# Performance work log

Hardware: AMD Instinct MI355X
Metric: run time of the kernel (lower is better)

The kernel has to match this reference:

```python
import jax, jax.numpy as jnp
import numpy as np

COMMITMENT_COST = 0.25
EMBEDDING_COST = 1.0


def setup_inputs() -> dict:
    key = jax.random.key(0)
    k1, k2 = jax.random.split(key)
    x = jax.random.normal(k1, (64, 1024, 64), dtype=jnp.float32)
    embeddings = jax.random.normal(k2, (1024, 64), dtype=jnp.float32)
    return {"x": x, "embeddings": embeddings}


def reference(x, embeddings):
    D = embeddings.shape[1]
    flat_x = x.reshape(-1, D)  # [N, D]
    distances = (
        jnp.sum(flat_x ** 2, axis=1, keepdims=True)
        + jnp.sum(embeddings ** 2, axis=1)
        - 2.0 * flat_x @ embeddings.T
    )
    encoding_indices = jnp.argmin(distances, axis=1)  # [N]
    quantized = embeddings[encoding_indices].reshape(x.shape)
    q_latent_loss = jnp.mean((quantized - jax.lax.stop_gradient(x)) ** 2) * EMBEDDING_COST
    e_latent_loss = jnp.mean((x - jax.lax.stop_gradient(quantized)) ** 2) * COMMITMENT_COST
    loss = q_latent_loss + e_latent_loss
    # Straight-through estimator
    quantized_st = x + jax.lax.stop_gradient(quantized - x)
    return (quantized_st, loss)
```

## Files before the change

kernel.cpp:

```cpp
#include <hip/hip_runtime.h>
#include <math.h>

#define NROWS 65536
#define D 64
#define K 1024
#define BR 128
#define EC 128
#define NCH 8
#define THREADS 256
#define TAU_S 0.005f
#define LOSS_SCALE (1.25f / (65536.0f * 64.0f))

typedef short bf16x8 __attribute__((ext_vector_type(8)));
typedef float f32x4 __attribute__((ext_vector_type(4)));

__device__ inline unsigned short f2bf(float f) {
    unsigned int u = __float_as_uint(f);
    unsigned int r = u + 0x7fffu + ((u >> 16) & 1u);
    return (unsigned short)(r >> 16);
}
__device__ inline float bf2f(unsigned short h) {
    return __uint_as_float(((unsigned int)h) << 16);
}
__device__ inline void cvt8(const float4& a, const float4& b, bf16x8& h, bf16x8& l) {
    float f[8] = {a.x, a.y, a.z, a.w, b.x, b.y, b.z, b.w};
#pragma unroll
    for (int j = 0; j < 8; ++j) {
        unsigned short hb = f2bf(f[j]);
        h[j] = (short)hb;
        l[j] = (short)f2bf(f[j] - bf2f(hb));
    }
}

#define MFMA __builtin_amdgcn_mfma_f32_16x16x32_bf16

__global__ void vq_prep(const float* __restrict__ E, float* __restrict__ Ch,
                        bf16x8* __restrict__ Eswz, float* __restrict__ lossp) {
    int k = blockIdx.x * blockDim.x + threadIdx.x;
    if (k == 0) *lossp = 0.f;
    if (k >= K) return;
    const float4* ev = (const float4*)(E + (size_t)k * D);
    float4 v4[16];
    float s = 0.f;
#pragma unroll
    for (int p = 0; p < 16; ++p) {
        float4 v = ev[p];
        v4[p] = v;
        s = fmaf(v.x, v.x, s); s = fmaf(v.y, v.y, s);
        s = fmaf(v.z, v.z, s); s = fmaf(v.w, v.w, s);
    }
    Ch[k] = 0.5f * s;
    int ch = k >> 7, c = k & 127, cs = c & 7;
    size_t base = (size_t)ch * 2048 + c * 8;
#pragma unroll
    for (int u8 = 0; u8 < 8; ++u8) {
        bf16x8 h, l;
        cvt8(v4[2 * u8], v4[2 * u8 + 1], h, l);
        Eswz[base + (u8 ^ cs)] = h;
        Eswz[base + 1024 + (u8 ^ cs)] = l;
    }
}

__global__ __launch_bounds__(THREADS, 2) void vq_main(
    const float* __restrict__ X, const float* __restrict__ E,
    const float* __restrict__ Chg, const bf16x8* __restrict__ Eswz,
    float* __restrict__ out, float* __restrict__ lossp)
{
    __shared__ bf16x8 sBuf[2][2048];
    __shared__ float  sCh[K];
    __shared__ int    sIdx[BR];
    __shared__ int    sFlag[BR];
    __shared__ int    sNf;
    __shared__ float  sLoss[4];

    const int t    = threadIdx.x;
    const int w    = t >> 6;
    const int lane = t & 63;
    const int l15  = lane & 15;
    const int l4   = lane >> 4;
    const int cs   = l15 & 7;
    const int o0   = l4 ^ cs;
    const int o1   = (4 + l4) ^ cs;

    const float4* Xg4 = (const float4*)X;
    const float4* Eg4 = (const float4*)E;

    if (t == 0) sNf = 0;
#pragma unroll
    for (int p = 0; p < 4; ++p) sCh[p * 256 + t] = Chg[p * 256 + t];

    bf16x8 ah[2][2], al[2][2];
#pragma unroll
    for (int rt = 0; rt < 2; ++rt) {
        size_t ab = ((size_t)blockIdx.x * BR + w * 32 + rt * 16 + l15) * 16;
#pragma unroll
        for (int kt = 0; kt < 2; ++kt) {
            float4 fa = Xg4[ab + kt * 8 + l4 * 2];
            float4 fb = Xg4[ab + kt * 8 + l4 * 2 + 1];
            cvt8(fa, fb, ah[rt][kt], al[rt][kt]);
        }
    }

    bf16x8 rs[8];
#pragma unroll
    for (int p = 0; p < 8; ++p) rs[p] = Eswz[p * 256 + t];
#pragma unroll
    for (int p = 0; p < 8; ++p) sBuf[0][p * 256 + t] = rs[p];
    __syncthreads();

    float m[2][4], m2[2][4]; int bk[2][4];
#pragma unroll
    for (int rt = 0; rt < 2; ++rt)
#pragma unroll
        for (int r = 0; r < 4; ++r) { m[rt][r] = -INFINITY; m2[rt][r] = -INFINITY; bk[rt][r] = 0; }

    for (int ch = 0; ch < NCH; ++ch) {
        const int cur = ch & 1;
        if (ch + 1 < NCH) {
#pragma unroll
            for (int p = 0; p < 8; ++p)
                rs[p] = Eswz[(size_t)(ch + 1) * 2048 + p * 256 + t];
        }
        const bf16x8* __restrict__ bufH = sBuf[cur];
        const bf16x8* __restrict__ bufL = sBuf[cur] + 1024;

#pragma unroll
        for (int g = 0; g < 4; ++g) {
            const int c0 = g * 32 + l15;
            const int c1 = c0 + 16;
            float ce0 = sCh[ch * EC + c0];
            float ce1 = sCh[ch * EC + c1];
            bf16x8 bh00 = bufH[c0 * 8 + o0];
            bf16x8 bh01 = bufH[c0 * 8 + o1];
            bf16x8 bl00 = bufL[c0 * 8 + o0];
            bf16x8 bl01 = bufL[c0 * 8 + o1];
            bf16x8 bh10 = bufH[c1 * 8 + o0];
            bf16x8 bh11 = bufH[c1 * 8 + o1];
            bf16x8 bl10 = bufL[c1 * 8 + o0];
            bf16x8 bl11 = bufL[c1 * 8 + o1];

            f32x4 a00 = {-ce0, -ce0, -ce0, -ce0};
            f32x4 a01 = {-ce0, -ce0, -ce0, -ce0};
            f32x4 a10 = {-ce1, -ce1, -ce1, -ce1};
            f32x4 a11 = {-ce1, -ce1, -ce1, -ce1};

            __builtin_amdgcn_s_setprio(1);
            a00 = MFMA(ah[0][0], bh00, a00, 0, 0, 0); a01 = MFMA(ah[1][0], bh00, a01, 0, 0, 0);
            a10 = MFMA(ah[0][0], bh10, a10, 0, 0, 0); a11 = MFMA(ah[1][0], bh10, a11, 0, 0, 0);
            a00 = MFMA(ah[0][1], bh01, a00, 0, 0, 0); a01 = MFMA(ah[1][1], bh01, a01, 0, 0, 0);
            a10 = MFMA(ah[0][1], bh11, a10, 0, 0, 0); a11 = MFMA(ah[1][1], bh11, a11, 0, 0, 0);
            a00 = MFMA(al[0][0], bh00, a00, 0, 0, 0); a01 = MFMA(al[1][0], bh00, a01, 0, 0, 0);
            a10 = MFMA(al[0][0], bh10, a10, 0, 0, 0); a11 = MFMA(al[1][0], bh10, a11, 0, 0, 0);
            a00 = MFMA(al[0][1], bh01, a00, 0, 0, 0); a01 = MFMA(al[1][1], bh01, a01, 0, 0, 0);
            a10 = MFMA(al[0][1], bh11, a10, 0, 0, 0); a11 = MFMA(al[1][1], bh11, a11, 0, 0, 0);
            a00 = MFMA(ah[0][0], bl00, a00, 0, 0, 0); a01 = MFMA(ah[1][0], bl00, a01, 0, 0, 0);
            a10 = MFMA(ah[0][0], bl10, a10, 0, 0, 0); a11 = MFMA(ah[1][0], bl10, a11, 0, 0, 0);
            a00 = MFMA(ah[0][1], bl01, a00, 0, 0, 0); a01 = MFMA(ah[1][1], bl01, a01, 0, 0, 0);
            a10 = MFMA(ah[0][1], bl11, a10, 0, 0, 0); a11 = MFMA(ah[1][1], bl11, a11, 0, 0, 0);
            __builtin_amdgcn_s_setprio(0);

            const int k0 = ch * EC + c0;
            const int k1 = ch * EC + c1;
#pragma unroll
            for (int r = 0; r < 4; ++r) {
                float v;
                v = a00[r];
                m2[0][r] = fmaxf(m2[0][r], fminf(m[0][r], v));
                bk[0][r] = (v > m[0][r]) ? k0 : bk[0][r];
                m[0][r]  = fmaxf(m[0][r], v);
                v = a01[r];
                m2[1][r] = fmaxf(m2[1][r], fminf(m[1][r], v));
                bk[1][r] = (v > m[1][r]) ? k0 : bk[1][r];
                m[1][r]  = fmaxf(m[1][r], v);
                v = a10[r];
                m2[0][r] = fmaxf(m2[0][r], fminf(m[0][r], v));
                bk[0][r] = (v > m[0][r]) ? k1 : bk[0][r];
                m[0][r]  = fmaxf(m[0][r], v);
                v = a11[r];
                m2[1][r] = fmaxf(m2[1][r], fminf(m[1][r], v));
                bk[1][r] = (v > m[1][r]) ? k1 : bk[1][r];
                m[1][r]  = fmaxf(m[1][r], v);
            }
        }

        if (ch + 1 < NCH) {
#pragma unroll
            for (int p = 0; p < 8; ++p) sBuf[cur ^ 1][p * 256 + t] = rs[p];
        }
        __syncthreads();
    }

#pragma unroll
    for (int rt = 0; rt < 2; ++rt)
#pragma unroll
        for (int r = 0; r < 4; ++r) {
            float mm = m[rt][r], mm2 = m2[rt][r]; int kk = bk[rt][r];
#pragma unroll
            for (int off = 1; off < 16; off <<= 1) {
                float om  = __shfl_xor(mm,  off, 64);
                float om2 = __shfl_xor(mm2, off, 64);
                int   ok  = __shfl_xor(kk,  off, 64);
                mm2 = fmaxf(fmaxf(mm2, om2), fminf(mm, om));
                if (om > mm || (om == mm && ok < kk)) { mm = om; kk = ok; }
            }
            if (l15 == 0) {
                int lr = w * 32 + rt * 16 + l4 * 4 + r;
                sIdx[lr] = kk;
                if (mm - mm2 < TAU_S) {
                    int pos = atomicAdd(&sNf, 1);
                    sFlag[pos] = lr;
                }
            }
        }
    __syncthreads();

    {
        int nf = sNf;
        for (int i = w; i < nf; i += 4) {
            int lr = sFlag[i];
            size_t grow = (size_t)blockIdx.x * BR + lr;
            const float4* xr = Xg4 + grow * 16;
            float bs = -INFINITY; int bki = 0;
#pragma unroll 1
            for (int jj = 0; jj < 16; ++jj) {
                int kq = jj * 64 + lane;
                const float4* er = Eg4 + (size_t)kq * 16;
                float a0 = 0.f, a1 = 0.f, a2 = 0.f, a3 = 0.f;
#pragma unroll
                for (int p = 0; p < 16; p += 4) {
                    float4 xv0 = xr[p],     e0 = er[p];
                    float4 xv1 = xr[p + 1], e1 = er[p + 1];
                    float4 xv2 = xr[p + 2], e2 = er[p + 2];
                    float4 xv3 = xr[p + 3], e3 = er[p + 3];
                    a0 = fmaf(xv0.x, e0.x, a0); a0 = fmaf(xv0.y, e0.y, a0);
                    a0 = fmaf(xv0.z, e0.z, a0); a0 = fmaf(xv0.w, e0.w, a0);
                    a1 = fmaf(xv1.x, e1.x, a1); a1 = fmaf(xv1.y, e1.y, a1);
                    a1 = fmaf(xv1.z, e1.z, a1); a1 = fmaf(xv1.w, e1.w, a1);
                    a2 = fmaf(xv2.x, e2.x, a2); a2 = fmaf(xv2.y, e2.y, a2);
                    a2 = fmaf(xv2.z, e2.z, a2); a2 = fmaf(xv2.w, e2.w, a2);
                    a3 = fmaf(xv3.x, e3.x, a3); a3 = fmaf(xv3.y, e3.y, a3);
                    a3 = fmaf(xv3.z, e3.z, a3); a3 = fmaf(xv3.w, e3.w, a3);
                }
                float sv = ((a0 + a1) + (a2 + a3)) - sCh[kq];
                if (sv > bs) { bs = sv; bki = kq; }
            }
#pragma unroll
            for (int off = 1; off < 64; off <<= 1) {
                float ob = __shfl_xor(bs, off, 64);
                int  okk = __shfl_xor(bki, off, 64);
                if (ob > bs || (ob == bs && okk < bki)) { bs = ob; bki = okk; }
            }
            if (lane == 0) sIdx[lr] = bki;
        }
    }
    __syncthreads();

    {
        int row = t >> 1, half = t & 1;
        int kb = sIdx[row];
        size_t grow = (size_t)blockIdx.x * BR + row;
        const float4* eq   = Eg4 + (size_t)kb * 16;
        const float4* xrow = Xg4 + grow * 16;
        float4* orow = (float4*)out + grow * 16;
        float ls = 0.f;
#pragma unroll
        for (int j = 0; j < 8; ++j) {
            int u = half * 8 + j;
            float4 qv = eq[u];
            float4 xv = xrow[u];
            orow[u] = qv;
            float dx = qv.x - xv.x; ls = fmaf(dx, dx, ls);
            float dy = qv.y - xv.y; ls = fmaf(dy, dy, ls);
            float dz = qv.z - xv.z; ls = fmaf(dz, dz, ls);
            float dw = qv.w - xv.w; ls = fmaf(dw, dw, ls);
        }
#pragma unroll
        for (int off = 32; off > 0; off >>= 1) ls += __shfl_down(ls, off, 64);
        if (lane == 0) sLoss[w] = ls;
        __syncthreads();
        if (t == 0)
            atomicAdd(lossp, (sLoss[0] + sLoss[1] + sLoss[2] + sLoss[3]) * LOSS_SCALE);
    }
}

extern "C" void kernel_launch(void* const* d_in, const int* in_sizes, int n_in,
                              void* d_out, int out_size, void* d_ws, size_t ws_size,
                              hipStream_t stream) {
    const float* X = (const float*)d_in[0];
    const float* E = (const float*)d_in[1];
    float* out   = (float*)d_out;
    float* lossp = out + (size_t)NROWS * D;

    float*  Ch   = (float*)d_ws;
    bf16x8* Eswz = (bf16x8*)((float*)d_ws + 1024);

    vq_prep<<<(K + 255) / 256, 256, 0, stream>>>(E, Ch, Eswz, lossp);

    vq_main<<<NROWS / BR, THREADS, 0, stream>>>(
        X, E, Ch, Eswz, out, lossp);
}
```

Measured before the change: 72.34 us.

## Stream MFMA-fragment-ordered codebook from global memory, split codebook across waves

The prep kernel now writes the bf16 hi/lo codebook directly in per-lane MFMA fragment order, so the main kernel loads B operands straight from global/L2 instead of staging chunks through double-buffered LDS with barriers. Block rows drop to 64 and each pair of waves splits the 1024 codes in half, merging top-1/top-2 through small LDS arrays; occupancy hint rises to 4 blocks. Per-block loss reduction becomes a per-wave atomic. This removes LDS traffic and per-chunk syncs but relies on L2 bandwidth for the codebook reads, doubles the number of blocks re-reading it, and increases global atomics on the loss.

```diff
diff --git a/kernel.cpp b/kernel.cpp
--- a/kernel.cpp
+++ b/kernel.cpp
@@ -4,9 +4,7 @@
 #define NROWS 65536
 #define D 64
 #define K 1024
-#define BR 128
-#define EC 128
-#define NCH 8
+#define BR 64
 #define THREADS 256
 #define TAU_S 0.005f
 #define LOSS_SCALE (1.25f / (65536.0f * 64.0f))
@@ -50,49 +48,46 @@
         s = fmaf(v.z, v.z, s); s = fmaf(v.w, v.w, s);
     }
     Ch[k] = 0.5f * s;
-    int ch = k >> 7, c = k & 127, cs = c & 7;
-    size_t base = (size_t)ch * 2048 + c * 8;
-#pragma unroll
-    for (int u8 = 0; u8 < 8; ++u8) {
-        bf16x8 h, l;
-        cvt8(v4[2 * u8], v4[2 * u8 + 1], h, l);
-        Eswz[base + (u8 ^ cs)] = h;
-        Eswz[base + 1024 + (u8 ^ cs)] = l;
-    }
-}
-
-__global__ __launch_bounds__(THREADS, 2) void vq_main(
+    int ct = k >> 4, li = k & 15;
+#pragma unroll
+    for (int kt = 0; kt < 2; ++kt)
+#pragma unroll
+        for (int o = 0; o < 4; ++o) {
+            int lane = li + 16 * o;
+            bf16x8 h, l;
+            cvt8(v4[kt * 8 + o * 2], v4[kt * 8 + o * 2 + 1], h, l);
+            Eswz[(size_t)(ct * 4 + kt * 2 + 0) * 64 + lane] = h;
+            Eswz[(size_t)(ct * 4 + kt * 2 + 1) * 64 + lane] = l;
+        }
+}
+
+__global__ __launch_bounds__(THREADS, 4) void vq_main(
     const float* __restrict__ X, const float* __restrict__ E,
     const float* __restrict__ Chg, const bf16x8* __restrict__ Eswz,
     float* __restrict__ out, float* __restrict__ lossp)
 {
-    __shared__ bf16x8 sBuf[2][2048];
-    __shared__ float  sCh[K];
-    __shared__ int    sIdx[BR];
-    __shared__ int    sFlag[BR];
-    __shared__ int    sNf;
-    __shared__ float  sLoss[4];
+    __shared__ float sM[2][BR], sM2[2][BR];
+    __shared__ int   sK[2][BR];
+    __shared__ int   sIdx[BR], sFlag[BR];
+    __shared__ int   sNf;
 
     const int t    = threadIdx.x;
     const int w    = t >> 6;
     const int lane = t & 63;
     const int l15  = lane & 15;
     const int l4   = lane >> 4;
-    const int cs   = l15 & 7;
-    const int o0   = l4 ^ cs;
-    const int o1   = (4 + l4) ^ cs;
+    const int rg   = w >> 1;
+    const int half = w & 1;
+
+    if (t == 0) sNf = 0;
 
     const float4* Xg4 = (const float4*)X;
     const float4* Eg4 = (const float4*)E;
 
-    if (t == 0) sNf = 0;
-#pragma unroll
-    for (int p = 0; p < 4; ++p) sCh[p * 256 + t] = Chg[p * 256 + t];
-
     bf16x8 ah[2][2], al[2][2];
 #pragma unroll
     for (int rt = 0; rt < 2; ++rt) {
-        size_t ab = ((size_t)blockIdx.x * BR + w * 32 + rt * 16 + l15) * 16;
+        size_t ab = ((size_t)blockIdx.x * BR + rg * 32 + rt * 16 + l15) * 16;
 #pragma unroll
         for (int kt = 0; kt < 2; ++kt) {
             float4 fa = Xg4[ab + kt * 8 + l4 * 2];
@@ -101,93 +96,67 @@
         }
     }
 
-    bf16x8 rs[8];
-#pragma unroll
-    for (int p = 0; p < 8; ++p) rs[p] = Eswz[p * 256 + t];
-#pragma unroll
-    for (int p = 0; p < 8; ++p) sBuf[0][p * 256 + t] = rs[p];
-    __syncthreads();
-
     float m[2][4], m2[2][4]; int bk[2][4];
 #pragma unroll
     for (int rt = 0; rt < 2; ++rt)
 #pragma unroll
         for (int r = 0; r < 4; ++r) { m[rt][r] = -INFINITY; m2[rt][r] = -INFINITY; bk[rt][r] = 0; }
 
-    for (int ch = 0; ch < NCH; ++ch) {
-        const int cur = ch & 1;
-        if (ch + 1 < NCH) {
-#pragma unroll
-            for (int p = 0; p < 8; ++p)
-                rs[p] = Eswz[(size_t)(ch + 1) * 2048 + p * 256 + t];
-        }
-        const bf16x8* __restrict__ bufH = sBuf[cur];
-        const bf16x8* __restrict__ bufL = sBuf[cur] + 1024;
-
-#pragma unroll
-        for (int g = 0; g < 4; ++g) {
-            const int c0 = g * 32 + l15;
-            const int c1 = c0 + 16;
-            float ce0 = sCh[ch * EC + c0];
-            float ce1 = sCh[ch * EC + c1];
-            bf16x8 bh00 = bufH[c0 * 8 + o0];
-            bf16x8 bh01 = bufH[c0 * 8 + o1];
-            bf16x8 bl00 = bufL[c0 * 8 + o0];
-            bf16x8 bl01 = bufL[c0 * 8 + o1];
-            bf16x8 bh10 = bufH[c1 * 8 + o0];
-            bf16x8 bh11 = bufH[c1 * 8 + o1];
-            bf16x8 bl10 = bufL[c1 * 8 + o0];
-            bf16x8 bl11 = bufL[c1 * 8 + o1];
-
-            f32x4 a00 = {-ce0, -ce0, -ce0, -ce0};
-            f32x4 a01 = {-ce0, -ce0, -ce0, -ce0};
-            f32x4 a10 = {-ce1, -ce1, -ce1, -ce1};
-            f32x4 a11 = {-ce1, -ce1, -ce1, -ce1};
-
-            __builtin_amdgcn_s_setprio(1);
-            a00 = MFMA(ah[0][0], bh00, a00, 0, 0, 0); a01 = MFMA(ah[1][0], bh00, a01, 0, 0, 0);
-            a10 = MFMA(ah[0][0], bh10, a10, 0, 0, 0); a11 = MFMA(ah[1][0], bh10, a11, 0, 0, 0);
-            a00 = MFMA(ah[0][1], bh01, a00, 0, 0, 0); a01 = MFMA(ah[1][1], bh01, a01, 0, 0, 0);
-            a10 = MFMA(ah[0][1], bh11, a10, 0, 0, 0); a11 = MFMA(ah[1][1], bh11, a11, 0, 0, 0);
-            a00 = MFMA(al[0][0], bh00, a00, 0, 0, 0); a01 = MFMA(al[1][0], bh00, a01, 0, 0, 0);
-            a10 = MFMA(al[0][0], bh10, a10, 0, 0, 0); a11 = MFMA(al[1][0], bh10, a11, 0, 0, 0);
-            a00 = MFMA(al[0][1], bh01, a00, 0, 0, 0); a01 = MFMA(al[1][1], bh01, a01, 0, 0, 0);
-            a10 = MFMA(al[0][1], bh11, a10, 0, 0, 0); a11 = MFMA(al[1][1], bh11, a11, 0, 0, 0);
-            a00 = MFMA(ah[0][0], bl00, a00, 0, 0, 0); a01 = MFMA(ah[1][0], bl00, a01, 0, 0, 0);
-            a10 = MFMA(ah[0][0], bl10, a10, 0, 0, 0); a11 = MFMA(ah[1][0], bl10, a11, 0, 0, 0);
-            a00 = MFMA(ah[0][1], bl01, a00, 0, 0, 0); a01 = MFMA(ah[1][1], bl01, a01, 0, 0, 0);
-            a10 = MFMA(ah[0][1], bl11, a10, 0, 0, 0); a11 = MFMA(ah[1][1], bl11, a11, 0, 0, 0);
-            __builtin_amdgcn_s_setprio(0);
-
-            const int k0 = ch * EC + c0;
-            const int k1 = ch * EC + c1;
-#pragma unroll
-            for (int r = 0; r < 4; ++r) {
-                float v;
-                v = a00[r];
-                m2[0][r] = fmaxf(m2[0][r], fminf(m[0][r], v));
-                bk[0][r] = (v > m[0][r]) ? k0 : bk[0][r];
-                m[0][r]  = fmaxf(m[0][r], v);
-                v = a01[r];
-                m2[1][r] = fmaxf(m2[1][r], fminf(m[1][r], v));
-                bk[1][r] = (v > m[1][r]) ? k0 : bk[1][r];
-                m[1][r]  = fmaxf(m[1][r], v);
-                v = a10[r];
-                m2[0][r] = fmaxf(m2[0][r], fminf(m[0][r], v));
-                bk[0][r] = (v > m[0][r]) ? k1 : bk[0][r];
-                m[0][r]  = fmaxf(m[0][r], v);
-                v = a11[r];
-                m2[1][r] = fmaxf(m2[1][r], fminf(m[1][r], v));
-                bk[1][r] = (v > m[1][r]) ? k1 : bk[1][r];
-                m[1][r]  = fmaxf(m[1][r], v);
-            }
-        }
-
-        if (ch + 1 < NCH) {
-#pragma unroll
-            for (int p = 0; p < 8; ++p) sBuf[cur ^ 1][p * 256 + t] = rs[p];
-        }
-        __syncthreads();
+    const int ctbase = half * 32;
+
+#pragma unroll 2
+    for (int g = 0; g < 16; ++g) {
+        const int ct0 = ctbase + g * 2;
+        const int ct1 = ct0 + 1;
+        const bf16x8* B0 = Eswz + (size_t)ct0 * 256 + lane;
+        const bf16x8* B1 = Eswz + (size_t)ct1 * 256 + lane;
+        bf16x8 bh00 = B0[0],   bl00 = B0[64];
+        bf16x8 bh01 = B0[128], bl01 = B0[192];
+        bf16x8 bh10 = B1[0],   bl10 = B1[64];
+        bf16x8 bh11 = B1[128], bl11 = B1[192];
+        float ce0 = Chg[ct0 * 16 + l15];
+        float ce1 = Chg[ct1 * 16 + l15];
+
+        f32x4 a00 = {-ce0, -ce0, -ce0, -ce0};
+        f32x4 a01 = {-ce0, -ce0, -ce0, -ce0};
+        f32x4 a10 = {-ce1, -ce1, -ce1, -ce1};
+        f32x4 a11 = {-ce1, -ce1, -ce1, -ce1};
+
+        a00 = MFMA(ah[0][0], bh00, a00, 0, 0, 0); a01 = MFMA(ah[1][0], bh00, a01, 0, 0, 0);
+        a10 = MFMA(ah[0][0], bh10, a10, 0, 0, 0); a11 = MFMA(ah[1][0], bh10, a11, 0, 0, 0);
+        a00 = MFMA(ah[0][1], bh01, a00, 0, 0, 0); a01 = MFMA(ah[1][1], bh01, a01, 0, 0, 0);
+        a10 = MFMA(ah[0][1], bh11, a10, 0, 0, 0); a11 = MFMA(ah[1][1], bh11, a11, 0, 0, 0);
+        a00 = MFMA(al[0][0], bh00, a00, 0, 0, 0); a01 = MFMA(al[1][0], bh00, a01, 0, 0, 0);
+        a10 = MFMA(al[0][0], bh10, a10, 0, 0, 0); a11 = MFMA(al[1][0], bh10, a11, 0, 0, 0);
+        a00 = MFMA(al[0][1], bh01, a00, 0, 0, 0); a01 = MFMA(al[1][1], bh01, a01, 0, 0, 0);
+        a10 = MFMA(al[0][1], bh11, a10, 0, 0, 0); a11 = MFMA(al[1][1], bh11, a11, 0, 0, 0);
+        a00 = MFMA(ah[0][0], bl00, a00, 0, 0, 0); a01 = MFMA(ah[1][0], bl00, a01, 0, 0, 0);
+        a10 = MFMA(ah[0][0], bl10, a10, 0, 0, 0); a11 = MFMA(ah[1][0], bl10, a11, 0, 0, 0);
+        a00 = MFMA(ah[0][1], bl01, a00, 0, 0, 0); a01 = MFMA(ah[1][1], bl01, a01, 0, 0, 0);
+        a10 = MFMA(ah[0][1], bl11, a10, 0, 0, 0); a11 = MFMA(ah[1][1], bl11, a11, 0, 0, 0);
+
+        const int k0 = ct0 * 16 + l15;
+        const int k1 = ct1 * 16 + l15;
+#pragma unroll
+        for (int r = 0; r < 4; ++r) {
+            float v;
+            v = a00[r];
+            m2[0][r] = fmaxf(m2[0][r], fminf(m[0][r], v));
+            bk[0][r] = (v > m[0][r]) ? k0 : bk[0][r];
+            m[0][r]  = fmaxf(m[0][r], v);
+            v = a01[r];
+            m2[1][r] = fmaxf(m2[1][r], fminf(m[1][r], v));
+            bk[1][r] = (v > m[1][r]) ? k0 : bk[1][r];
+            m[1][r]  = fmaxf(m[1][r], v);
+            v = a10[r];
+            m2[0][r] = fmaxf(m2[0][r], fminf(m[0][r], v));
+            bk[0][r] = (v > m[0][r]) ? k1 : bk[0][r];
+            m[0][r]  = fmaxf(m[0][r], v);
+            v = a11[r];
+            m2[1][r] = fmaxf(m2[1][r], fminf(m[1][r], v));
+            bk[1][r] = (v > m[1][r]) ? k1 : bk[1][r];
+            m[1][r]  = fmaxf(m[1][r], v);
+        }
     }
 
 #pragma unroll
@@ -204,14 +173,24 @@
                 if (om > mm || (om == mm && ok < kk)) { mm = om; kk = ok; }
             }
             if (l15 == 0) {
-                int lr = w * 32 + rt * 16 + l4 * 4 + r;
-                sIdx[lr] = kk;
-                if (mm - mm2 < TAU_S) {
-                    int pos = atomicAdd(&sNf, 1);
-                    sFlag[pos] = lr;
-                }
-            }
-        }
+                int lr = rg * 32 + rt * 16 + l4 * 4 + r;
+                sM[half][lr] = mm; sM2[half][lr] = mm2; sK[half][lr] = kk;
+            }
+        }
+    __syncthreads();
+
+    if (t < BR) {
+        float mA = sM[0][t], mB = sM[1][t];
+        int   kA = sK[0][t], kB = sK[1][t];
+        float top = fmaxf(mA, mB);
+        int   kk  = (mB > mA) ? kB : kA;
+        float sec = fmaxf(fmaxf(sM2[0][t], sM2[1][t]), fminf(mA, mB));
+        sIdx[t] = kk;
+        if (top - sec < TAU_S) {
+            int pos = atomicAdd(&sNf, 1);
+            sFlag[pos] = t;
+        }
+    }
     __syncthreads();
 
     {
@@ -241,7 +220,7 @@
                     a3 = fmaf(xv3.x, e3.x, a3); a3 = fmaf(xv3.y, e3.y, a3);
                     a3 = fmaf(xv3.z, e3.z, a3); a3 = fmaf(xv3.w, e3.w, a3);
                 }
-                float sv = ((a0 + a1) + (a2 + a3)) - sCh[kq];
+                float sv = ((a0 + a1) + (a2 + a3)) - Chg[kq];
                 if (sv > bs) { bs = sv; bki = kq; }
             }
 #pragma unroll
@@ -256,7 +235,7 @@
     __syncthreads();
 
     {
-        int row = t >> 1, half = t & 1;
+        int row = t >> 2, q = t & 3;
         int kb = sIdx[row];
         size_t grow = (size_t)blockIdx.x * BR + row;
         const float4* eq   = Eg4 + (size_t)kb * 16;
@@ -264,8 +243,8 @@
         float4* orow = (float4*)out + grow * 16;
         float ls = 0.f;
 #pragma unroll
-        for (int j = 0; j < 8; ++j) {
-            int u = half * 8 + j;
+        for (int j = 0; j < 4; ++j) {
+            int u = q * 4 + j;
             float4 qv = eq[u];
             float4 xv = xrow[u];
             orow[u] = qv;
@@ -276,10 +255,7 @@
         }
 #pragma unroll
         for (int off = 32; off > 0; off >>= 1) ls += __shfl_down(ls, off, 64);
-        if (lane == 0) sLoss[w] = ls;
-        __syncthreads();
-        if (t == 0)
-            atomicAdd(lossp, (sLoss[0] + sLoss[1] + sLoss[2] + sLoss[3]) * LOSS_SCALE);
+        if (lane == 0) atomicAdd(lossp, ls * LOSS_SCALE);
     }
 }
 
```

Measured after the change: 100.2 us. 1.39x slower.
